# Optimization experiments

Hardware: AMD Instinct MI355X
Metric: run time of the kernel (lower is better)

Reference implementation:

```python
import jax, jax.numpy as jnp
import numpy as np
from jax import lax

# Lens/aperture geometry (must match init_kwargs lens_mask)
LENS = 21
RADIUS = LENS // 2
EPS = 1e-8


def _offsets():
    """Flattened 21x21 aperture footprint: distance kernel, circular lens mask,
    and (row, col) slice offsets into the padded image."""
    ys, xs = np.meshgrid(np.arange(LENS), np.arange(LENS), indexing='ij')
    dy = ys - RADIUS
    dx = xs - RADIUS
    dist = np.sqrt(dy * dy + dx * dx).astype(np.float32)
    mask = (dist <= RADIUS).astype(np.float32)
    return (jnp.asarray(dist.ravel()), jnp.asarray(mask.ravel()),
            jnp.asarray(ys.ravel().astype(np.int32)),
            jnp.asarray(xs.ravel().astype(np.int32)))


def scatter_layer(x5, lens_effect):
    """Scatter (splat) defocus rendering of one RGBAD layer.

    x5: [B,5,H,W] (r,g,b,alpha,relative-disparity); lens_effect: [B,1].
    Each source pixel splats its premultiplied color over a disk of radius
    r = |disp| * lens_effect (soft-edged, area-normalized). Because the disk
    kernel is symmetric in the offset, the scatter is computed as a gather
    over the 21x21 footprint with weights taken from the *source* pixel.

    Returns [B,5,H,W]: [:3] accumulated rgb, [3] accumulated weight,
    [4] occupancy (clipped accumulated alpha-weight).
    """
    B, _, H, W = x5.shape
    dist, mask, oy, ox = _offsets()
    rgb, a, disp = x5[:, :3], x5[:, 3:4], x5[:, 4:5]
    r = jnp.clip(jnp.abs(disp) * lens_effect[:, :, None, None], 0.0, float(RADIUS))  # [B,1,H,W]

    # per-source-pixel soft disk area: sum_o mask(o) * clip(r + 0.5 - dist(o), 0, 1)
    def area_step(acc, dm):
        d, m = dm
        return acc + m * jnp.clip(r + 0.5 - d, 0.0, 1.0), None

    area, _ = lax.scan(area_step, jnp.zeros_like(r), (dist, mask))

    # premultiplied source energy, normalized by splat area
    s = jnp.concatenate([rgb * a, a], axis=1) / (area + EPS)  # [B,4,H,W]
    pad = ((0, 0), (0, 0), (RADIUS, RADIUS), (RADIUS, RADIUS))
    s_pad = jnp.pad(s, pad)
    r_pad = jnp.pad(r, pad)

    # gather formulation of the scatter: out[q] = sum_o s[q-o] * w(o; r[q-o])
    def step(acc, dmyx):
        d, m, dy, dx = dmyx
        sl = lax.dynamic_slice(s_pad, (0, 0, dy, dx), (B, 4, H, W))
        rsl = lax.dynamic_slice(r_pad, (0, 0, dy, dx), (B, 1, H, W))
        w = m * jnp.clip(rsl + 0.5 - d, 0.0, 1.0)
        return acc + sl * w, None

    out4, _ = lax.scan(step, jnp.zeros((B, 4, H, W), x5.dtype), (dist, mask, oy, ox))
    occu = jnp.clip(out4[:, 3:4], 0.0, 1.0)
    return jnp.concatenate([out4, occu], axis=1)


def setup_inputs() -> dict:
    key = jax.random.key(0)
    k1, k2 = jax.random.split(key)
    B, N_LAYER, H, W = 2, 3, 512, 512
    rgbad_layers = jax.random.uniform(k1, (B, 5 * N_LAYER, H, W), dtype=jnp.float32)
    # lens strength in a range that exercises the full 21x21 footprint
    lens_effect = jax.random.uniform(k2, (B, 1), dtype=jnp.float32) * 10.0
    focal = jnp.zeros((B, 5 * N_LAYER, H, W), dtype=jnp.float32)
    return {"rgbad_layers": rgbad_layers, "lens_effect": lens_effect, "focal": focal}


def reference(rgbad_layers, lens_effect, focal):
    """Multi_Layer_Renderer.forward: front-to-back alpha compositing of
    per-layer scatter-rendered bokeh."""
    x = rgbad_layers - focal
    n_layer = x.shape[1] // 5
    blurs = [scatter_layer(x[:, 5 * i:5 * (i + 1)], lens_effect) for i in range(n_layer)]
    rgb0, w0, o0 = blurs[0][:, :3], blurs[0][:, 3:4], blurs[0][:, 4:5]
    blur_rgb = rgb0 / (w0 + EPS) * o0
    trans = 1.0 - o0  # accumulated transmittance
    for li in range(1, n_layer):
        lr, lw, lo = blurs[li][:, :3], blurs[li][:, 3:4], blurs[li][:, 4:5]
        blur_rgb = blur_rgb + lr / (lw + EPS) * (trans * lo)
        trans = trans * (1.0 - lo)
    return blur_rgb
```

## Files before the change

kernel.cpp:

```cpp
#include <hip/hip_runtime.h>
#include <hip/hip_bf16.h>

#define HH 512
#define WW 512
#define HWSZ (512*512)

typedef _Float16 hh4 __attribute__((ext_vector_type(4)));
typedef _Float16 hh2 __attribute__((ext_vector_type(2)));
typedef float    ff4 __attribute__((ext_vector_type(4)));

__device__ __forceinline__ float clamp01(float x) {
    return __builtin_amdgcn_fmed3f(x, 0.0f, 1.0f);
}

__global__ __launch_bounds__(256, 2)
void mlr_fused_kernel(const float* __restrict__ rgbad,
                      const float* __restrict__ lens_eff,
                      const float* __restrict__ focal,
                      float* __restrict__ out,
                      int nbx, int B)
{
    constexpr int TW = 64, TH = 16;
    constexpr int SW = 88;
    constexpr int SH = TH + 20;
    constexpr int LP = 90;
    constexpr int NG = SW / 4;
    constexpr int NSLOT = SH * NG;
    constexpr int NIT = (NSLOT + 255) / 256;

    __shared__ uint2 sP[SH * LP];
    __shared__ uint  rP[SH * LP / 2];
    __shared__ int   maxbits;

    const int tx  = threadIdx.x;
    const int ty  = threadIdx.y;
    const int tid = ty * 16 + tx;
    const int bid = blockIdx.x;
    const int bb  = bid % B;
    const int t   = bid / B;
    const int bx0 = (t % nbx) * TW;
    const int by0 = (t / nbx) * TH;
    const float lens = lens_eff[bb];

    static constexpr float DJ[44] = {
        0.f, 1.f, 1.41421356f, 2.f, 2.23606798f, 2.82842712f, 3.f, 3.16227766f,
        3.60555128f, 4.f, 4.12310563f, 4.24264069f, 4.47213595f, 5.f, 5.09901951f,
        5.38516481f, 5.65685425f, 5.83095189f, 6.f, 6.08276253f, 6.32455532f,
        6.40312424f, 6.70820393f, 7.f, 7.07106781f, 7.21110255f, 7.28010989f,
        7.61577311f, 7.81024968f, 8.f, 8.06225775f, 8.24621125f, 8.48528137f,
        8.54400375f, 8.60232527f, 8.94427191f, 9.f, 9.05538514f, 9.21954446f,
        9.43398113f, 9.48683298f, 9.84885780f, 9.89949494f, 10.f };
    static constexpr float CNT[44] = {
        1,4,4,4,8,4,4,8,8,4,8,4,8,12,8,8,4,8,4,8,8,8,
        8,4,12,8,8,8,8,4,16,8,4,8,8,8,4,8,16,8,8,8,4,12 };

    float blurR[4] = {0,0,0,0}, blurG[4] = {0,0,0,0}, blurB[4] = {0,0,0,0};
    float trans[4] = {1,1,1,1};

#pragma unroll 1
    for (int l = 0; l < 3; ++l) {
        __syncthreads();
        if (tid == 0) maxbits = 0;
        __syncthreads();

        const float* pin = rgbad + (size_t)(bb * 15 + 5 * l) * HWSZ;
        const float* pfo = focal + (size_t)(bb * 15 + 5 * l) * HWSZ;
        float mloc = 0.f;

#pragma unroll
        for (int it = 0; it < NIT; ++it) {
            int s = tid + it * 256;
            s = (s < NSLOT) ? s : (NSLOT - 1);
            const int row = s / NG;
            const int grp = s - row * NG;
            const int gy  = by0 - 10 + row;
            const int gx0 = bx0 - 12 + 4 * grp;

            ff4 i0 = {0,0,0,0}, i1 = {0,0,0,0}, i2 = {0,0,0,0}, i3 = {0,0,0,0}, i4 = {0,0,0,0};
            ff4 f0 = {0,0,0,0}, f1 = {0,0,0,0}, f2 = {0,0,0,0}, f3 = {0,0,0,0}, f4 = {0,0,0,0};
            const bool valid = ((unsigned)gy < (unsigned)HH) && ((unsigned)gx0 < (unsigned)WW);
            if (valid) {
                const size_t off = (size_t)gy * WW + (size_t)gx0;
                i0 = *reinterpret_cast<const ff4*>(pin + off);
                i1 = *reinterpret_cast<const ff4*>(pin + off +   HWSZ);
                i2 = *reinterpret_cast<const ff4*>(pin + off + 2*HWSZ);
                i3 = *reinterpret_cast<const ff4*>(pin + off + 3*HWSZ);
                i4 = *reinterpret_cast<const ff4*>(pin + off + 4*HWSZ);
                f0 = *reinterpret_cast<const ff4*>(pfo + off);
                f1 = *reinterpret_cast<const ff4*>(pfo + off +   HWSZ);
                f2 = *reinterpret_cast<const ff4*>(pfo + off + 2*HWSZ);
                f3 = *reinterpret_cast<const ff4*>(pfo + off + 3*HWSZ);
                f4 = *reinterpret_cast<const ff4*>(pfo + off + 4*HWSZ);
            }
            uint2 pk[4];
            unsigned short rh[4];
#pragma unroll
            for (int k = 0; k < 4; ++k) {
                const float cr = i0[k] - f0[k];
                const float cg = i1[k] - f1[k];
                const float cb = i2[k] - f2[k];
                const float ca = i3[k] - f3[k];
                const float cd = i4[k] - f4[k];
                const float r  = fminf(fabsf(cd) * lens, 10.f);
                const float rp05 = r + 0.5f;
                float a0 = 0.f, a1 = 0.f;
#pragma unroll
                for (int j = 0; j < 44; j += 2) {
                    a0 = fmaf(CNT[j],     clamp01(rp05 - DJ[j]),     a0);
                    a1 = fmaf(CNT[j + 1], clamp01(rp05 - DJ[j + 1]), a1);
                }
                const float inv = 1.0f / (a0 + a1 + 1e-8f);
                const float pa  = ca * inv;
                hh4 hv;
                hv.x = (_Float16)(cr * pa);
                hv.y = (_Float16)(cg * pa);
                hv.z = (_Float16)(cb * pa);
                hv.w = (_Float16)pa;
                pk[k] = __builtin_bit_cast(uint2, hv);
                rh[k] = __builtin_bit_cast(unsigned short, (_Float16)rp05);
                mloc  = fmaxf(mloc, rp05);
            }
            const int base = row * LP + 4 * grp;
            uint4 s01, s23;
            s01.x = pk[0].x; s01.y = pk[0].y; s01.z = pk[1].x; s01.w = pk[1].y;
            s23.x = pk[2].x; s23.y = pk[2].y; s23.z = pk[3].x; s23.w = pk[3].y;
            *reinterpret_cast<uint4*>(&sP[base])     = s01;
            *reinterpret_cast<uint4*>(&sP[base + 2]) = s23;
            uint2 rr;
            rr.x = (uint)rh[0] | ((uint)rh[1] << 16);
            rr.y = (uint)rh[2] | ((uint)rh[3] << 16);
            *reinterpret_cast<uint2*>(&rP[base >> 1]) = rr;
        }
        atomicMax(&maxbits, __float_as_int(mloc));
        __syncthreads();

        const float rmax = __int_as_float(maxbits);
        const int U = min(10, (int)ceilf(rmax) - 1);

        float accR[4] = {0,0,0,0}, accG[4] = {0,0,0,0};
        float accB[4] = {0,0,0,0}, accW[4] = {0,0,0,0};

#define TAP1(vv, sw0, sw1, rpf) { \
            uint2 sw; sw.x = (sw0); sw.y = (sw1); \
            const hh4 hv = __builtin_bit_cast(hh4, sw); \
            const float s0 = (float)hv.x, s1 = (float)hv.y; \
            const float s2 = (float)hv.z, s3 = (float)hv.w; \
            _Pragma("unroll") \
            for (int ox = 0; ox < 4; ++ox) { \
                const int dx = (vv) - ox; \
                if (dx >= -10 && dx <= 10) { \
                    const float w = clamp01((rpf) - dd[dx + 10]); \
                    accR[ox] = fmaf(s0, w, accR[ox]); \
                    accG[ox] = fmaf(s1, w, accG[ox]); \
                    accB[ox] = fmaf(s2, w, accB[ox]); \
                    accW[ox] = fmaf(s3, w, accW[ox]); } } }

#define PAIR(v0) { \
            const uint4 sp = *reinterpret_cast<const uint4*>(&sP[rbase + (v0)]); \
            const hh2 rp2 = __builtin_bit_cast(hh2, rP[(rbase + (v0)) >> 1]); \
            TAP1((v0),     sp.x, sp.y, (float)rp2.x); \
            TAP1((v0) + 1, sp.z, sp.w, (float)rp2.y); }

#pragma unroll 1
        for (int u = -U; u <= U; ++u) {
            const float u2f = (float)(u * u);
            const float vm2 = rmax * rmax - u2f;
            float dd[21];
#pragma unroll
            for (int k = 0; k < 21; ++k) {
                const int dxk = k - 10;
                const float q = u2f + (float)(dxk * dxk);
                dd[k] = (q <= 100.0f) ? __builtin_sqrtf(q) : 1e9f;
            }
            const int rbase = (ty + 10 + u) * LP + 12 + 4 * tx;

            PAIR(-2) PAIR(0) PAIR(2) PAIR(4)
            if (vm2 > 9.0f)  { PAIR(-6) PAIR(-4) PAIR(6) PAIR(8) }
            if (vm2 > 36.0f) { PAIR(-8) PAIR(10) }
            if (vm2 > 81.0f) { PAIR(-10) PAIR(12) }
        }
#undef PAIR
#undef TAP1

#pragma unroll
        for (int ox = 0; ox < 4; ++ox) {
            const float wsum = accW[ox];
            const float occ  = clamp01(wsum);
            const float f    = trans[ox] * occ / (wsum + 1e-8f);
            blurR[ox] = fmaf(accR[ox], f, blurR[ox]);
            blurG[ox] = fmaf(accG[ox], f, blurG[ox]);
            blurB[ox] = fmaf(accB[ox], f, blurB[ox]);
            trans[ox] *= (1.0f - occ);
        }
    }

    const int oy = by0 + ty;
    const size_t obase = (size_t)bb * 3 * HWSZ + (size_t)oy * WW + (size_t)(bx0 + 4 * tx);

    float4 vR, vG, vB;
    vR.x = blurR[0]; vR.y = blurR[1]; vR.z = blurR[2]; vR.w = blurR[3];
    vG.x = blurG[0]; vG.y = blurG[1]; vG.z = blurG[2]; vG.w = blurG[3];
    vB.x = blurB[0]; vB.y = blurB[1]; vB.z = blurB[2]; vB.w = blurB[3];

    *reinterpret_cast<float4*>(out + obase)            = vR;
    *reinterpret_cast<float4*>(out + obase + HWSZ)     = vG;
    *reinterpret_cast<float4*>(out + obase + 2 * HWSZ) = vB;
}

extern "C" void kernel_launch(void* const* d_in, const int* in_sizes, int n_in,
                              void* d_out, int out_size, void* d_ws, size_t ws_size,
                              hipStream_t stream) {
    const float* rgbad = (const float*)d_in[0];
    const float* lens  = (const float*)d_in[1];
    const float* focal = (const float*)d_in[2];
    float* out = (float*)d_out;
    const int B = in_sizes[1];
    const int nbx = WW / 64;
    const int nby = HH / 16;
    dim3 grid(nbx * nby * B, 1, 1);
    dim3 block(16, 16, 1);
    hipLaunchKernelGGL(mlr_fused_kernel, grid, block, 0, stream,
                       rgbad, lens, focal, out, nbx, B);
}
```

Baseline: 46.30 us.

## Use packed fp16 weights and fdot2 accumulation in gather and area loops

The inner gather loop now computes tap weights two taps at a time in packed half precision, using a precomputed fp16 distance-pair table. Each pair of taps is accumulated into fp32 with v_dot2 instructions. Channel values are reorganized with byte permutes so R, G, B and A each form one half2 operand. The per-pixel area sum uses the same fdot2 path. This roughly halves the VALU ops per tap, but the clamp and weights are computed in fp16, so some precision is lost.

```diff
diff --git a/kernel.cpp b/kernel.cpp
--- a/kernel.cpp
+++ b/kernel.cpp
@@ -11,6 +11,14 @@
 
 __device__ __forceinline__ float clamp01(float x) {
     return __builtin_amdgcn_fmed3f(x, 0.0f, 1.0f);
+}
+__device__ __forceinline__ hh2 clamp01h2(hh2 x) {
+    const hh2 z = {(_Float16)0.0f, (_Float16)0.0f};
+    const hh2 o = {(_Float16)1.0f, (_Float16)1.0f};
+    return __builtin_elementwise_min(__builtin_elementwise_max(x, z), o);
+}
+__device__ __forceinline__ hh2 pkrtz(float a, float b) {
+    return __builtin_bit_cast(hh2, __builtin_amdgcn_cvt_pkrtz(a, b));
 }
 
 __global__ __launch_bounds__(256, 2)
@@ -103,13 +111,16 @@
                 const float cd = i4[k] - f4[k];
                 const float r  = fminf(fabsf(cd) * lens, 10.f);
                 const float rp05 = r + 0.5f;
-                float a0 = 0.f, a1 = 0.f;
+                const hh2 rp2s = pkrtz(rp05, rp05);
+                float aacc = 0.f;
 #pragma unroll
                 for (int j = 0; j < 44; j += 2) {
-                    a0 = fmaf(CNT[j],     clamp01(rp05 - DJ[j]),     a0);
-                    a1 = fmaf(CNT[j + 1], clamp01(rp05 - DJ[j + 1]), a1);
+                    const hh2 dj2 = {(_Float16)DJ[j], (_Float16)DJ[j + 1]};
+                    const hh2 c2  = {(_Float16)CNT[j], (_Float16)CNT[j + 1]};
+                    const hh2 w2  = clamp01h2(rp2s - dj2);
+                    aacc = __builtin_amdgcn_fdot2(w2, c2, aacc, false);
                 }
-                const float inv = 1.0f / (a0 + a1 + 1e-8f);
+                const float inv = 1.0f / (aacc + 1e-8f);
                 const float pa  = ca * inv;
                 hh4 hv;
                 hv.x = (_Float16)(cr * pa);
@@ -126,10 +137,10 @@
             s23.x = pk[2].x; s23.y = pk[2].y; s23.z = pk[3].x; s23.w = pk[3].y;
             *reinterpret_cast<uint4*>(&sP[base])     = s01;
             *reinterpret_cast<uint4*>(&sP[base + 2]) = s23;
-            uint2 rr;
-            rr.x = (uint)rh[0] | ((uint)rh[1] << 16);
-            rr.y = (uint)rh[2] | ((uint)rh[3] << 16);
-            *reinterpret_cast<uint2*>(&rP[base >> 1]) = rr;
+            uint2 rr2;
+            rr2.x = (uint)rh[0] | ((uint)rh[1] << 16);
+            rr2.y = (uint)rh[2] | ((uint)rh[3] << 16);
+            *reinterpret_cast<uint2*>(&rP[base >> 1]) = rr2;
         }
         atomicMax(&maxbits, __float_as_int(mloc));
         __syncthreads();
@@ -140,47 +151,44 @@
         float accR[4] = {0,0,0,0}, accG[4] = {0,0,0,0};
         float accB[4] = {0,0,0,0}, accW[4] = {0,0,0,0};
 
-#define TAP1(vv, sw0, sw1, rpf) { \
-            uint2 sw; sw.x = (sw0); sw.y = (sw1); \
-            const hh4 hv = __builtin_bit_cast(hh4, sw); \
-            const float s0 = (float)hv.x, s1 = (float)hv.y; \
-            const float s2 = (float)hv.z, s3 = (float)hv.w; \
+#define PAIRD(v0) { \
+            const uint4 sp = *reinterpret_cast<const uint4*>(&sP[rbase + (v0)]); \
+            const hh2 rp2 = __builtin_bit_cast(hh2, rP[(rbase + (v0)) >> 1]); \
+            const hh2 cR = __builtin_bit_cast(hh2, __builtin_amdgcn_perm(sp.z, sp.x, 0x05040100u)); \
+            const hh2 cG = __builtin_bit_cast(hh2, __builtin_amdgcn_perm(sp.z, sp.x, 0x07060302u)); \
+            const hh2 cB = __builtin_bit_cast(hh2, __builtin_amdgcn_perm(sp.w, sp.y, 0x05040100u)); \
+            const hh2 cA = __builtin_bit_cast(hh2, __builtin_amdgcn_perm(sp.w, sp.y, 0x07060302u)); \
             _Pragma("unroll") \
             for (int ox = 0; ox < 4; ++ox) { \
-                const int dx = (vv) - ox; \
-                if (dx >= -10 && dx <= 10) { \
-                    const float w = clamp01((rpf) - dd[dx + 10]); \
-                    accR[ox] = fmaf(s0, w, accR[ox]); \
-                    accG[ox] = fmaf(s1, w, accG[ox]); \
-                    accB[ox] = fmaf(s2, w, accB[ox]); \
-                    accW[ox] = fmaf(s3, w, accW[ox]); } } }
-
-#define PAIR(v0) { \
-            const uint4 sp = *reinterpret_cast<const uint4*>(&sP[rbase + (v0)]); \
-            const hh2 rp2 = __builtin_bit_cast(hh2, rP[(rbase + (v0)) >> 1]); \
-            TAP1((v0),     sp.x, sp.y, (float)rp2.x); \
-            TAP1((v0) + 1, sp.z, sp.w, (float)rp2.y); }
+                const hh2 w2 = clamp01h2(rp2 - hdd2[(v0) - ox + 13]); \
+                accR[ox] = __builtin_amdgcn_fdot2(cR, w2, accR[ox], false); \
+                accG[ox] = __builtin_amdgcn_fdot2(cG, w2, accG[ox], false); \
+                accB[ox] = __builtin_amdgcn_fdot2(cB, w2, accB[ox], false); \
+                accW[ox] = __builtin_amdgcn_fdot2(cA, w2, accW[ox], false); \
+            } }
 
 #pragma unroll 1
         for (int u = -U; u <= U; ++u) {
             const float u2f = (float)(u * u);
             const float vm2 = rmax * rmax - u2f;
-            float dd[21];
-#pragma unroll
-            for (int k = 0; k < 21; ++k) {
-                const int dxk = k - 10;
-                const float q = u2f + (float)(dxk * dxk);
-                dd[k] = (q <= 100.0f) ? __builtin_sqrtf(q) : 1e9f;
+            hh2 hdd2[26];
+#pragma unroll
+            for (int m = 0; m < 26; ++m) {
+                const int dxa = m - 13, dxb = dxa + 1;
+                const float qa = u2f + (float)(dxa * dxa);
+                const float qb = u2f + (float)(dxb * dxb);
+                const float da = (qa <= 100.0f) ? __builtin_sqrtf(qa) : 3000.0f;
+                const float db = (qb <= 100.0f) ? __builtin_sqrtf(qb) : 3000.0f;
+                hdd2[m] = pkrtz(da, db);
             }
             const int rbase = (ty + 10 + u) * LP + 12 + 4 * tx;
 
-            PAIR(-2) PAIR(0) PAIR(2) PAIR(4)
-            if (vm2 > 9.0f)  { PAIR(-6) PAIR(-4) PAIR(6) PAIR(8) }
-            if (vm2 > 36.0f) { PAIR(-8) PAIR(10) }
-            if (vm2 > 81.0f) { PAIR(-10) PAIR(12) }
+            PAIRD(-2) PAIRD(0) PAIRD(2) PAIRD(4)
+            if (vm2 > 9.0f)  { PAIRD(-6) PAIRD(-4) PAIRD(6) PAIRD(8) }
+            if (vm2 > 36.0f) { PAIRD(-8) PAIRD(10) }
+            if (vm2 > 81.0f) { PAIRD(-10) PAIRD(12) }
         }
-#undef PAIR
-#undef TAP1
+#undef PAIRD
 
 #pragma unroll
         for (int ox = 0; ox < 4; ++ox) {
```

Result: faster. 43.99 us (-5.0%).
